# Kernel tuning notes

Measured on AMD Instinct MI355X. Metric: run time of the kernel, lower is better.

Reference implementation:

```python
import jax, jax.numpy as jnp
import numpy as np

VOCAB = 50000
DIM = 300
BATCH = 1024
CTX = 10


def setup_inputs() -> dict:
    key = jax.random.key(0)
    k1, k2, k3, k4 = jax.random.split(key, 4)
    context = jax.random.randint(k1, (BATCH, CTX), 0, VOCAB, dtype=jnp.int64 if jax.config.read('jax_enable_x64') else jnp.int32)
    W_proj = jax.random.normal(k2, (DIM, VOCAB), dtype=jnp.float32) * 0.02
    W_cls = jax.random.normal(k3, (VOCAB, DIM), dtype=jnp.float32) * 0.02
    b_cls = jax.random.normal(k4, (VOCAB,), dtype=jnp.float32) * 0.02
    return {"context": context, "W_proj": W_proj, "W_cls": W_cls, "b_cls": b_cls, "pad_idx": 0}


def reference(context, W_proj, W_cls, b_cls, pad_idx):
    # One-hot @ W_proj.T == gather of W_proj columns at context ids: [B, C, D]
    emb = jnp.take(W_proj, context, axis=1)            # [D, B, C]
    emb = jnp.moveaxis(emb, 0, -1)                     # [B, C, D]
    # zeroing the pad_idx column of the one-hot kills pad tokens' contribution,
    # but the mean still divides by the full context length C.
    mask = (context != pad_idx).astype(emb.dtype)      # [B, C]
    emb = emb * mask[..., None]
    pooled = emb.mean(axis=1)                          # [B, D]
    logits = pooled @ W_cls.T + b_cls                  # [B, V]
    return jax.nn.log_softmax(logits, axis=1)
```

## Files before the change

### kernel.cpp

```cpp
#include <hip/hip_runtime.h>
#include <math.h>

#define B_SZ 1024
#define CTXL 10
#define DIM  300
#define VOC  50000
#define KP   320
#define BM   128
#define BN   128
#define BK   64
#define NTIL 391
#define NSG  50
#define WROW 1200
#define WMAXOFF 59999984

typedef short s16x8 __attribute__((ext_vector_type(8)));
typedef float f32x4 __attribute__((ext_vector_type(4)));
typedef _Float16 h4 __attribute__((ext_vector_type(4)));

__device__ __forceinline__ void gload_lds16(const void* g, void* lds) {
  __builtin_amdgcn_global_load_lds((const __attribute__((address_space(1))) void*)g,
                                   (__attribute__((address_space(3))) void*)lds, 16, 0, 0);
}

__global__ void transpose_kernel(const float* __restrict__ W, float* __restrict__ WT) {
  __shared__ float tile[32][33];
  const int v0 = blockIdx.x * 32, d0 = blockIdx.y * 32;
  const int tx = threadIdx.x & 31, ty = threadIdx.x >> 5;
#pragma unroll
  for (int i = 0; i < 32; i += 8) {
    const int d = d0 + ty + i, v = v0 + tx;
    tile[ty + i][tx] = (d < DIM && v < VOC) ? W[d * VOC + v] : 0.f;
  }
  __syncthreads();
#pragma unroll
  for (int i = 0; i < 32; i += 8) {
    const int v = v0 + ty + i, d = d0 + tx;
    if (v < VOC && d < DIM) WT[v * DIM + d] = tile[tx][ty + i];
  }
}

__global__ void pool_kernel(const int* __restrict__ ctx, const float* __restrict__ WT,
                            const int* __restrict__ padp, __bf16* __restrict__ pooled) {
  const int b = blockIdx.x;
  const int d = threadIdx.x;
  const int pad = *padp;
  float s = 0.f;
  if (d < DIM) {
#pragma unroll
    for (int c = 0; c < CTXL; ++c) {
      const int id = ctx[b * CTXL + c];
      if (id != pad) s += WT[id * DIM + d];
    }
  }
  pooled[b * KP + d] = (__bf16)(s * 0.1f);
}

__global__ __launch_bounds__(256, 3) void gemm_kernel(const __bf16* __restrict__ A,
                                                      const float* __restrict__ Wcls,
                                                      const float* __restrict__ bias,
                                                      float* __restrict__ out) {
  __shared__ __align__(16) char smem[49152];
  const int bid = blockIdx.x;
  const int s = bid & 7;
  const int mj = (bid >> 3) & 7;
  const int G = bid >> 6;
  const int nt = G * 8 + s;
  if (nt >= NTIL) return;
  const int m0 = mj * BM;
  const int n0 = nt * BN;
  const int t = threadIdx.x;
  const int lane = t & 63;
  const int wave = t >> 6;
  const int wm = wave >> 1, wn = wave & 1;

  f32x4 acc[4][4];
#pragma unroll
  for (int i = 0; i < 4; ++i)
#pragma unroll
    for (int j = 0; j < 4; ++j) acc[i][j] = (f32x4){0.f, 0.f, 0.f, 0.f};

  const char* Ab = (const char*)A;
  const char* Wb = (const char*)Wcls;
  char* bufA[2] = {smem, smem + 16384};
  char* bufB = smem + 32768;
  const int hi = lane >> 4;
  const int lr8 = lane >> 3;
  const int gcA = (lane & 7) ^ lr8;
  const int brow = t >> 1;
  const int bhalf = t & 1;
  int browg = n0 + brow; if (browg > VOC - 1) browg = VOC - 1;
  const long browoff = (long)browg * WROW;

#pragma unroll
  for (int i = 0; i < 4; ++i) {
    const int r = wave * 32 + i * 8 + lr8;
    gload_lds16(Ab + (m0 + r) * (KP * 2) + gcA * 16, bufA[0] + wave * 4096 + i * 1024);
  }
  {
    f32x4 breg[8];
#pragma unroll
    for (int j = 0; j < 8; ++j) {
      long off = browoff + (bhalf * 8 + j) * 16;
      if (off > WMAXOFF) off = WMAXOFF;
      breg[j] = *(const f32x4*)(Wb + off);
    }
#pragma unroll
    for (int jj = 0; jj < 4; ++jj) {
      union { __bf16 h; short v; } cv;
      s16x8 bb;
      cv.h = (__bf16)breg[jj * 2][0];     bb[0] = cv.v;
      cv.h = (__bf16)breg[jj * 2][1];     bb[1] = cv.v;
      cv.h = (__bf16)breg[jj * 2][2];     bb[2] = cv.v;
      cv.h = (__bf16)breg[jj * 2][3];     bb[3] = cv.v;
      cv.h = (__bf16)breg[jj * 2 + 1][0]; bb[4] = cv.v;
      cv.h = (__bf16)breg[jj * 2 + 1][1]; bb[5] = cv.v;
      cv.h = (__bf16)breg[jj * 2 + 1][2]; bb[6] = cv.v;
      cv.h = (__bf16)breg[jj * 2 + 1][3]; bb[7] = cv.v;
      const int c = bhalf * 4 + jj;
      *(s16x8*)(bufB + brow * 128 + ((c ^ (brow & 7)) * 16)) = bb;
    }
  }
  __syncthreads();

#pragma unroll
  for (int k = 0; k < 5; ++k) {
    char* bAc = bufA[k & 1];
    char* bAn = bufA[(k + 1) & 1];

    f32x4 breg[8];
    if (k < 4) {
      const int k0n = (k + 1) * BK;
#pragma unroll
      for (int i = 0; i < 4; ++i) {
        const int r = wave * 32 + i * 8 + lr8;
        gload_lds16(Ab + (m0 + r) * (KP * 2) + k0n * 2 + gcA * 16, bAn + wave * 4096 + i * 1024);
      }
#pragma unroll
      for (int j = 0; j < 8; ++j) {
        long off = browoff + (k0n / 4 + bhalf * 8 + j) * 16;
        if (off > WMAXOFF) off = WMAXOFF;
        breg[j] = *(const f32x4*)(Wb + off);
      }
    }

#pragma unroll
    for (int kk = 0; kk < 2; ++kk) {
      s16x8 af[4], bfr[4];
#pragma unroll
      for (int mf = 0; mf < 4; ++mf) {
        const int ra = wm * 64 + mf * 16 + (lane & 15);
        af[mf] = *(const s16x8*)(bAc + ra * 128 + (((kk * 4 + hi) ^ (ra & 7)) * 16));
      }
#pragma unroll
      for (int nf = 0; nf < 4; ++nf) {
        const int rb = wn * 64 + nf * 16 + (lane & 15);
        bfr[nf] = *(const s16x8*)(bufB + rb * 128 + (((kk * 4 + hi) ^ (rb & 7)) * 16));
      }
#pragma unroll
      for (int mf = 0; mf < 4; ++mf)
#pragma unroll
        for (int nf = 0; nf < 4; ++nf)
          acc[mf][nf] = __builtin_amdgcn_mfma_f32_16x16x32_bf16(af[mf], bfr[nf], acc[mf][nf], 0, 0, 0);
    }

    if (k < 4) {
      __syncthreads();
#pragma unroll
      for (int jj = 0; jj < 4; ++jj) {
        union { __bf16 h; short v; } cv;
        s16x8 bb;
        cv.h = (__bf16)breg[jj * 2][0];     bb[0] = cv.v;
        cv.h = (__bf16)breg[jj * 2][1];     bb[1] = cv.v;
        cv.h = (__bf16)breg[jj * 2][2];     bb[2] = cv.v;
        cv.h = (__bf16)breg[jj * 2][3];     bb[3] = cv.v;
        cv.h = (__bf16)breg[jj * 2 + 1][0]; bb[4] = cv.v;
        cv.h = (__bf16)breg[jj * 2 + 1][1]; bb[5] = cv.v;
        cv.h = (__bf16)breg[jj * 2 + 1][2]; bb[6] = cv.v;
        cv.h = (__bf16)breg[jj * 2 + 1][3]; bb[7] = cv.v;
        const int c = bhalf * 4 + jj;
        *(s16x8*)(bufB + brow * 128 + ((c ^ (brow & 7)) * 16)) = bb;
      }
      __syncthreads();
    }
  }

  const int cl = lane & 15, lg = lane >> 4;
#pragma unroll
  for (int nf = 0; nf < 4; ++nf) {
    const int col = n0 + wn * 64 + nf * 16 + cl;
    if (col < VOC) {
      const float bia = bias[col];
#pragma unroll
      for (int mf = 0; mf < 4; ++mf)
#pragma unroll
        for (int reg = 0; reg < 4; ++reg) {
          const int row = m0 + wm * 64 + mf * 16 + lg * 4 + reg;
          out[row * VOC + col] = acc[mf][nf][reg] + bia;
        }
    }
  }
}

__global__ __launch_bounds__(1024) void softfix_kernel(float* __restrict__ out) {
  extern __shared__ __align__(16) char stash[];
  __shared__ float red[17];
  const int b = blockIdx.x;
  const int tid = threadIdx.x;
  float4* rowp = (float4*)(out + b * VOC);
  h4* st = (h4*)stash;

  float s = 0.f;
  for (int i = tid; i < VOC / 4; i += 1024) {
    const float4 v = rowp[i];
    h4 h;
    h[0] = (_Float16)v.x; h[1] = (_Float16)v.y;
    h[2] = (_Float16)v.z; h[3] = (_Float16)v.w;
    st[i] = h;
    s += __expf(v.x) + __expf(v.y) + __expf(v.z) + __expf(v.w);
  }
#pragma unroll
  for (int off = 1; off < 64; off <<= 1) s += __shfl_xor(s, off, 64);
  if ((tid & 63) == 0) red[tid >> 6] = s;
  __syncthreads();
  float tot = 0.f;
#pragma unroll
  for (int j = 0; j < 16; ++j) tot += red[j];
  const float l = logf(tot);

  for (int i = tid; i < VOC / 4; i += 1024) {
    const h4 h = st[i];
    float4 o;
    o.x = (float)h[0] - l; o.y = (float)h[1] - l;
    o.z = (float)h[2] - l; o.w = (float)h[3] - l;
    rowp[i] = o;
  }
}

extern "C" void kernel_launch(void* const* d_in, const int* in_sizes, int n_in,
                              void* d_out, int out_size, void* d_ws, size_t ws_size,
                              hipStream_t stream) {
  (void)in_sizes; (void)n_in; (void)out_size;
  const int*   ctx   = (const int*)d_in[0];
  const float* Wproj = (const float*)d_in[1];
  const float* Wcls  = (const float*)d_in[2];
  const float* bcls  = (const float*)d_in[3];
  const int*   padp  = (const int*)d_in[4];
  float* out = (float*)d_out;

  if (ws_size < 655360) return;
  __bf16* pooled = (__bf16*)d_ws;
  float*  WT     = out;

  transpose_kernel<<<dim3(1563, 10), 256, 0, stream>>>(Wproj, WT);
  pool_kernel<<<B_SZ, KP, 0, stream>>>(ctx, WT, padp, pooled);
  gemm_kernel<<<NSG * 64, 256, 0, stream>>>(pooled, Wcls, bcls, out);
  softfix_kernel<<<B_SZ, 1024, 100352, stream>>>(out);
}
```

Before: 480.9 us.

## Drop LDS staging in GEMM and fp16 stash in log-softmax

The GEMM now loads A and B fragments straight from global memory into registers for each MFMA step. This removes the LDS double buffering, swizzling and all block barriers, at the cost of less data reuse across waves and more redundant global and L2 traffic. The log-softmax kernel no longer keeps an fp16 copy of the row in LDS and instead re-reads the row from global memory in its second pass. That removes the large dynamic shared allocation and the precision loss, but adds a second global read per row.

```diff
diff --git a/kernel.cpp b/kernel.cpp
--- a/kernel.cpp
+++ b/kernel.cpp
@@ -6,9 +6,6 @@
 #define DIM  300
 #define VOC  50000
 #define KP   320
-#define BM   128
-#define BN   128
-#define BK   64
 #define NTIL 391
 #define NSG  50
 #define WROW 1200
@@ -16,12 +13,6 @@
 
 typedef short s16x8 __attribute__((ext_vector_type(8)));
 typedef float f32x4 __attribute__((ext_vector_type(4)));
-typedef _Float16 h4 __attribute__((ext_vector_type(4)));
-
-__device__ __forceinline__ void gload_lds16(const void* g, void* lds) {
-  __builtin_amdgcn_global_load_lds((const __attribute__((address_space(1))) void*)g,
-                                   (__attribute__((address_space(3))) void*)lds, 16, 0, 0);
-}
 
 __global__ void transpose_kernel(const float* __restrict__ W, float* __restrict__ WT) {
   __shared__ float tile[32][33];
@@ -56,23 +47,24 @@
   pooled[b * KP + d] = (__bf16)(s * 0.1f);
 }
 
-__global__ __launch_bounds__(256, 3) void gemm_kernel(const __bf16* __restrict__ A,
+__global__ __launch_bounds__(256, 2) void gemm_kernel(const __bf16* __restrict__ A,
                                                       const float* __restrict__ Wcls,
                                                       const float* __restrict__ bias,
                                                       float* __restrict__ out) {
-  __shared__ __align__(16) char smem[49152];
   const int bid = blockIdx.x;
   const int s = bid & 7;
   const int mj = (bid >> 3) & 7;
   const int G = bid >> 6;
   const int nt = G * 8 + s;
   if (nt >= NTIL) return;
-  const int m0 = mj * BM;
-  const int n0 = nt * BN;
+  const int m0 = mj * 128;
+  const int n0 = nt * 128;
   const int t = threadIdx.x;
   const int lane = t & 63;
   const int wave = t >> 6;
   const int wm = wave >> 1, wn = wave & 1;
+  const int fr = lane & 15;
+  const int hi = lane >> 4;
 
   f32x4 acc[4][4];
 #pragma unroll
@@ -82,120 +74,64 @@
 
   const char* Ab = (const char*)A;
   const char* Wb = (const char*)Wcls;
-  char* bufA[2] = {smem, smem + 16384};
-  char* bufB = smem + 32768;
-  const int hi = lane >> 4;
-  const int lr8 = lane >> 3;
-  const int gcA = (lane & 7) ^ lr8;
-  const int brow = t >> 1;
-  const int bhalf = t & 1;
-  int browg = n0 + brow; if (browg > VOC - 1) browg = VOC - 1;
-  const long browoff = (long)browg * WROW;
+
+  int aoff[4];
+#pragma unroll
+  for (int mf = 0; mf < 4; ++mf)
+    aoff[mf] = (m0 + wm * 64 + mf * 16 + fr) * (KP * 2);
+  int boff[4];
+#pragma unroll
+  for (int nf = 0; nf < 4; ++nf) {
+    int r = n0 + wn * 64 + nf * 16 + fr;
+    if (r > VOC - 1) r = VOC - 1;
+    boff[nf] = r * WROW;
+  }
 
 #pragma unroll
-  for (int i = 0; i < 4; ++i) {
-    const int r = wave * 32 + i * 8 + lr8;
-    gload_lds16(Ab + (m0 + r) * (KP * 2) + gcA * 16, bufA[0] + wave * 4096 + i * 1024);
-  }
-  {
-    f32x4 breg[8];
+  for (int ks = 0; ks < 10; ++ks) {
+    const int koff = ks * 32 + hi * 8;
+    s16x8 af[4];
 #pragma unroll
-    for (int j = 0; j < 8; ++j) {
-      long off = browoff + (bhalf * 8 + j) * 16;
-      if (off > WMAXOFF) off = WMAXOFF;
-      breg[j] = *(const f32x4*)(Wb + off);
+    for (int mf = 0; mf < 4; ++mf)
+      af[mf] = *(const s16x8*)(Ab + aoff[mf] + koff * 2);
+    s16x8 bf[4];
+#pragma unroll
+    for (int nf = 0; nf < 4; ++nf) {
+      int o0 = boff[nf] + koff * 4;
+      int o1 = o0 + 16;
+      if (o0 > WMAXOFF) o0 = WMAXOFF;
+      if (o1 > WMAXOFF) o1 = WMAXOFF;
+      const f32x4 x0 = *(const f32x4*)(Wb + o0);
+      const f32x4 x1 = *(const f32x4*)(Wb + o1);
+      union { __bf16 h; short v; } cv;
+      s16x8 bb;
+      cv.h = (__bf16)x0[0]; bb[0] = cv.v;
+      cv.h = (__bf16)x0[1]; bb[1] = cv.v;
+      cv.h = (__bf16)x0[2]; bb[2] = cv.v;
+      cv.h = (__bf16)x0[3]; bb[3] = cv.v;
+      cv.h = (__bf16)x1[0]; bb[4] = cv.v;
+      cv.h = (__bf16)x1[1]; bb[5] = cv.v;
+      cv.h = (__bf16)x1[2]; bb[6] = cv.v;
+      cv.h = (__bf16)x1[3]; bb[7] = cv.v;
+      bf[nf] = bb;
     }
 #pragma unroll
-    for (int jj = 0; jj < 4; ++jj) {
-      union { __bf16 h; short v; } cv;
-      s16x8 bb;
-      cv.h = (__bf16)breg[jj * 2][0];     bb[0] = cv.v;
-      cv.h = (__bf16)breg[jj * 2][1];     bb[1] = cv.v;
-      cv.h = (__bf16)breg[jj * 2][2];     bb[2] = cv.v;
-      cv.h = (__bf16)breg[jj * 2][3];     bb[3] = cv.v;
-      cv.h = (__bf16)breg[jj * 2 + 1][0]; bb[4] = cv.v;
-      cv.h = (__bf16)breg[jj * 2 + 1][1]; bb[5] = cv.v;
-      cv.h = (__bf16)breg[jj * 2 + 1][2]; bb[6] = cv.v;
-      cv.h = (__bf16)breg[jj * 2 + 1][3]; bb[7] = cv.v;
-      const int c = bhalf * 4 + jj;
-      *(s16x8*)(bufB + brow * 128 + ((c ^ (brow & 7)) * 16)) = bb;
-    }
+    for (int mf = 0; mf < 4; ++mf)
+#pragma unroll
+      for (int nf = 0; nf < 4; ++nf)
+        acc[mf][nf] = __builtin_amdgcn_mfma_f32_16x16x32_bf16(af[mf], bf[nf], acc[mf][nf], 0, 0, 0);
   }
-  __syncthreads();
 
 #pragma unroll
-  for (int k = 0; k < 5; ++k) {
-    char* bAc = bufA[k & 1];
-    char* bAn = bufA[(k + 1) & 1];
-
-    f32x4 breg[8];
-    if (k < 4) {
-      const int k0n = (k + 1) * BK;
-#pragma unroll
-      for (int i = 0; i < 4; ++i) {
-        const int r = wave * 32 + i * 8 + lr8;
-        gload_lds16(Ab + (m0 + r) * (KP * 2) + k0n * 2 + gcA * 16, bAn + wave * 4096 + i * 1024);
-      }
-#pragma unroll
-      for (int j = 0; j < 8; ++j) {
-        long off = browoff + (k0n / 4 + bhalf * 8 + j) * 16;
-        if (off > WMAXOFF) off = WMAXOFF;
-        breg[j] = *(const f32x4*)(Wb + off);
-      }
-    }
-
-#pragma unroll
-    for (int kk = 0; kk < 2; ++kk) {
-      s16x8 af[4], bfr[4];
-#pragma unroll
-      for (int mf = 0; mf < 4; ++mf) {
-        const int ra = wm * 64 + mf * 16 + (lane & 15);
-        af[mf] = *(const s16x8*)(bAc + ra * 128 + (((kk * 4 + hi) ^ (ra & 7)) * 16));
-      }
-#pragma unroll
-      for (int nf = 0; nf < 4; ++nf) {
-        const int rb = wn * 64 + nf * 16 + (lane & 15);
-        bfr[nf] = *(const s16x8*)(bufB + rb * 128 + (((kk * 4 + hi) ^ (rb & 7)) * 16));
-      }
-#pragma unroll
-      for (int mf = 0; mf < 4; ++mf)
-#pragma unroll
-        for (int nf = 0; nf < 4; ++nf)
-          acc[mf][nf] = __builtin_amdgcn_mfma_f32_16x16x32_bf16(af[mf], bfr[nf], acc[mf][nf], 0, 0, 0);
-    }
-
-    if (k < 4) {
-      __syncthreads();
-#pragma unroll
-      for (int jj = 0; jj < 4; ++jj) {
-        union { __bf16 h; short v; } cv;
-        s16x8 bb;
-        cv.h = (__bf16)breg[jj * 2][0];     bb[0] = cv.v;
-        cv.h = (__bf16)breg[jj * 2][1];     bb[1] = cv.v;
-        cv.h = (__bf16)breg[jj * 2][2];     bb[2] = cv.v;
-        cv.h = (__bf16)breg[jj * 2][3];     bb[3] = cv.v;
-        cv.h = (__bf16)breg[jj * 2 + 1][0]; bb[4] = cv.v;
-        cv.h = (__bf16)breg[jj * 2 + 1][1]; bb[5] = cv.v;
-        cv.h = (__bf16)breg[jj * 2 + 1][2]; bb[6] = cv.v;
-        cv.h = (__bf16)breg[jj * 2 + 1][3]; bb[7] = cv.v;
-        const int c = bhalf * 4 + jj;
-        *(s16x8*)(bufB + brow * 128 + ((c ^ (brow & 7)) * 16)) = bb;
-      }
-      __syncthreads();
-    }
-  }
-
-  const int cl = lane & 15, lg = lane >> 4;
-#pragma unroll
   for (int nf = 0; nf < 4; ++nf) {
-    const int col = n0 + wn * 64 + nf * 16 + cl;
+    const int col = n0 + wn * 64 + nf * 16 + fr;
     if (col < VOC) {
       const float bia = bias[col];
 #pragma unroll
       for (int mf = 0; mf < 4; ++mf)
 #pragma unroll
         for (int reg = 0; reg < 4; ++reg) {
-          const int row = m0 + wm * 64 + mf * 16 + lg * 4 + reg;
+          const int row = m0 + wm * 64 + mf * 16 + hi * 4 + reg;
           out[row * VOC + col] = acc[mf][nf][reg] + bia;
         }
     }
@@ -203,20 +139,14 @@
 }
 
 __global__ __launch_bounds__(1024) void softfix_kernel(float* __restrict__ out) {
-  extern __shared__ __align__(16) char stash[];
-  __shared__ float red[17];
+  __shared__ float red[16];
   const int b = blockIdx.x;
   const int tid = threadIdx.x;
   float4* rowp = (float4*)(out + b * VOC);
-  h4* st = (h4*)stash;
 
   float s = 0.f;
   for (int i = tid; i < VOC / 4; i += 1024) {
     const float4 v = rowp[i];
-    h4 h;
-    h[0] = (_Float16)v.x; h[1] = (_Float16)v.y;
-    h[2] = (_Float16)v.z; h[3] = (_Float16)v.w;
-    st[i] = h;
     s += __expf(v.x) + __expf(v.y) + __expf(v.z) + __expf(v.w);
   }
 #pragma unroll
@@ -229,18 +159,17 @@
   const float l = logf(tot);
 
   for (int i = tid; i < VOC / 4; i += 1024) {
-    const h4 h = st[i];
-    float4 o;
-    o.x = (float)h[0] - l; o.y = (float)h[1] - l;
-    o.z = (float)h[2] - l; o.w = (float)h[3] - l;
-    rowp[i] = o;
+    float4 v = rowp[i];
+    v.x -= l; v.y -= l; v.z -= l; v.w -= l;
+    rowp[i] = v;
   }
 }
 
 extern "C" void kernel_launch(void* const* d_in, const int* in_sizes, int n_in,
                               void* d_out, int out_size, void* d_ws, size_t ws_size,
                               hipStream_t stream) {
-  (void)in_sizes; (void)n_in; (void)out_size;
+  (void)in_sizes; (void)out_size;
+  if (n_in < 5) return;
   const int*   ctx   = (const int*)d_in[0];
   const float* Wproj = (const float*)d_in[1];
   const float* Wcls  = (const float*)d_in[2];
@@ -255,5 +184,5 @@
   transpose_kernel<<<dim3(1563, 10), 256, 0, stream>>>(Wproj, WT);
   pool_kernel<<<B_SZ, KP, 0, stream>>>(ctx, WT, padp, pooled);
   gemm_kernel<<<NSG * 64, 256, 0, stream>>>(pooled, Wcls, bcls, out);
-  softfix_kernel<<<B_SZ, 1024, 100352, stream>>>(out);
+  softfix_kernel<<<B_SZ, 1024, 0, stream>>>(out);
 }
```

Measured after the change: 547.8 us. 13.9% more time.
